# Kernel tuning notes

Measured on AMD Instinct MI355X. Metric: run time of the kernel, lower is better.

Reference implementation:

```python
import jax, jax.numpy as jnp
import numpy as np

N = 100000
E = 800000
F_IN = 256
HID = 64
H = 4
NEG_SLOPE = 0.2
BN_EPS = 1e-5


def setup_inputs() -> dict:
    key = jax.random.key(0)
    ks = jax.random.split(key, 20)
    s = 0.05
    return {
        "x": jax.random.normal(ks[0], (N, F_IN), jnp.float32),
        "edge_index": jax.random.randint(ks[1], (2, E), 0, N, jnp.int64),
        # GCNConv params
        "W_gcn": jax.random.normal(ks[2], (F_IN, HID), jnp.float32) * s,
        "b_gcn": jnp.zeros((HID,), jnp.float32),
        "g0": jnp.ones((HID,), jnp.float32),
        "beta0": jnp.zeros((HID,), jnp.float32),
        # GATConv 1 params
        "W1": jax.random.normal(ks[3], (HID, H * HID), jnp.float32) * s,
        "a_src1": jax.random.normal(ks[4], (H, HID), jnp.float32) * s,
        "a_dst1": jax.random.normal(ks[5], (H, HID), jnp.float32) * s,
        "b1": jnp.zeros((H * HID,), jnp.float32),
        "g1": jnp.ones((H * HID,), jnp.float32),
        "beta1": jnp.zeros((H * HID,), jnp.float32),
        # GATConv 2 params
        "W2": jax.random.normal(ks[6], (H * HID, H * HID), jnp.float32) * s,
        "a_src2": jax.random.normal(ks[7], (H, HID), jnp.float32) * s,
        "a_dst2": jax.random.normal(ks[8], (H, HID), jnp.float32) * s,
        "b2": jnp.zeros((H * HID,), jnp.float32),
        "g2": jnp.ones((H * HID,), jnp.float32),
        "beta2": jnp.zeros((H * HID,), jnp.float32),
    }


def _add_self_loops(edge_index, n):
    loop = jnp.arange(n, dtype=edge_index.dtype)
    src = jnp.concatenate([edge_index[0], loop])
    dst = jnp.concatenate([edge_index[1], loop])
    return src, dst


def _batch_norm(x, g, b):
    # BatchNorm1d, training-mode batch stats (biased variance), no dropout
    m = x.mean(0)
    v = x.var(0)
    return g * (x - m) * jax.lax.rsqrt(v + BN_EPS) + b


def _gcn_conv(x, src, dst, W, b, n):
    # symmetric normalization with self-loops already included in src/dst
    deg = jax.ops.segment_sum(jnp.ones_like(dst, jnp.float32), dst, n)
    dinv = jax.lax.rsqrt(jnp.maximum(deg, 1.0))
    norm = dinv[src] * dinv[dst]  # [E']
    h = x @ W  # [N, HID]
    out = jax.ops.segment_sum(h[src] * norm[:, None], dst, n)
    return out + b


def _gat_conv(x, src, dst, W, a_src, a_dst, b, n):
    h = (x @ W).reshape(n, H, HID)  # [N, H, C]
    alpha_s = jnp.einsum("nhc,hc->nh", h, a_src)  # [N, H]
    alpha_d = jnp.einsum("nhc,hc->nh", h, a_dst)
    e = alpha_s[src] + alpha_d[dst]  # [E', H]
    e = jnp.where(e > 0, e, NEG_SLOPE * e)  # LeakyReLU
    # softmax over incoming edges of each dst node, per head
    emax = jax.ops.segment_max(e, dst, n)
    w = jnp.exp(e - emax[dst])
    wsum = jax.ops.segment_sum(w, dst, n)
    att = w / wsum[dst]  # [E', H]
    out = jax.ops.segment_sum(att[:, :, None] * h[src], dst, n)  # [N, H, C]
    return out.reshape(n, H * HID) + b


def reference(x, edge_index, W_gcn, b_gcn, g0, beta0, W1, a_src1, a_dst1, b1,
              g1, beta1, W2, a_src2, a_dst2, b2, g2, beta2):
    n = x.shape[0]
    src, dst = _add_self_loops(edge_index, n)
    h = jax.nn.relu(_gcn_conv(x, src, dst, W_gcn, b_gcn, n))
    h = _batch_norm(h, g0, beta0)
    h = _gat_conv(h, src, dst, W1, a_src1, a_dst1, b1, n)
    h = jax.nn.elu(_batch_norm(h, g1, beta1))
    h = _gat_conv(h, src, dst, W2, a_src2, a_dst2, b2, n)
    h = jax.nn.elu(_batch_norm(h, g2, beta2))
    return h
```

## Files before the change

kernel.cpp:

```cpp
#include <hip/hip_runtime.h>
#include <hip/hip_bf16.h>
#include <math.h>

#define NN 100000
#define EE 800000
#define FIN 256
#define CH 64
#define C1 256
#define BN_EPS 1e-5f
#define NEG_SLOPE 0.2f

typedef __attribute__((ext_vector_type(8))) short short8;
typedef __attribute__((ext_vector_type(8))) unsigned short u16x8;
typedef __attribute__((ext_vector_type(4))) float f32x4;

__device__ __forceinline__ float bf2f(ushort u) {
    return __uint_as_float(((unsigned)u) << 16);
}
__device__ __forceinline__ ushort f2bf(float f) {
    unsigned u = __float_as_uint(f);
    return (ushort)((u + 0x7FFF + ((u >> 16) & 1)) >> 16);
}

__global__ void hist_kernel(const int* __restrict__ ei, int* __restrict__ deg) {
    int t = blockIdx.x * 256 + threadIdx.x;
    if (t < EE) atomicAdd(&deg[ei[EE + t]], 1);
}
__global__ void dinv_kernel(const int* __restrict__ deg, float* __restrict__ dinv) {
    int i = blockIdx.x * 256 + threadIdx.x;
    if (i < NN) dinv[i] = rsqrtf((float)(deg[i] + 1));
}
__global__ void scan_k1(const int* __restrict__ deg, int* __restrict__ row_start,
                        int* __restrict__ bsum) {
    __shared__ int sh[256];
    int t = threadIdx.x;
    int i = blockIdx.x * 256 + t;
    int v = (i < NN) ? (deg[i] + 1) : 0;
    sh[t] = v;
    __syncthreads();
    for (int off = 1; off < 256; off <<= 1) {
        int add = (t >= off) ? sh[t - off] : 0;
        __syncthreads();
        sh[t] += add;
        __syncthreads();
    }
    if (i < NN) row_start[i] = sh[t] - v;
    if (t == 255) bsum[blockIdx.x] = sh[255];
}
__global__ void scan_k2(int* __restrict__ bsum, int nb) {
    __shared__ int sh[512];
    int t = threadIdx.x;
    int v = (t < nb) ? bsum[t] : 0;
    sh[t] = v;
    __syncthreads();
    for (int off = 1; off < 512; off <<= 1) {
        int add = (t >= off) ? sh[t - off] : 0;
        __syncthreads();
        sh[t] += add;
        __syncthreads();
    }
    if (t < nb) bsum[t] = sh[t] - v;
}
__global__ void scan_k3(int* __restrict__ row_start, const int* __restrict__ bsum) {
    int i = blockIdx.x * 256 + threadIdx.x;
    if (i < NN) row_start[i] += bsum[i >> 8];
    if (i == NN) row_start[NN] = EE + NN;
}
__global__ void scatter_kernel(const int* __restrict__ ei, const int* __restrict__ row_start,
                               int* __restrict__ fill, int* __restrict__ sorted) {
    int t = blockIdx.x * 256 + threadIdx.x;
    if (t >= EE + NN) return;
    int s, d;
    if (t < EE) { s = ei[t]; d = ei[EE + t]; }
    else        { s = t - EE; d = s; }
    int pos = atomicAdd(&fill[d], 1);
    sorted[row_start[d] + pos] = s;
}

__global__ void transpose_w(const float* __restrict__ W, ushort* __restrict__ Bt, int M, int K) {
    int idx = blockIdx.x * 256 + threadIdx.x;
    if (idx < M * K) {
        int m = idx / K, n = idx % K;
        Bt[n * M + m] = f2bf(W[idx]);
    }
}

__global__ __launch_bounds__(256) void gemm_mfma(
        const void* __restrict__ Ap, const ushort* __restrict__ Bt,
        ushort* __restrict__ C, int M, int K, int a_fp32,
        const float* __restrict__ a_src, const float* __restrict__ a_dst,
        float* __restrict__ alpha_s, float* __restrict__ alpha_d) {
    __shared__ ushort As[64][40];
    __shared__ ushort Bs[64][40];
    int t = threadIdx.x;
    int w = t >> 6;
    int l = t & 63;
    int rowBase = blockIdx.y * 64;
    int colBase = blockIdx.x * 64;
    int srow = t >> 2;
    int sk = (t & 3) * 8;
    int m = l & 15, q = l >> 4;
    f32x4 acc[4] = {};
    for (int k0 = 0; k0 < M; k0 += 32) {
        int gr = rowBase + srow;
        if (a_fp32) {
            ushort4 u0 = {0, 0, 0, 0}, u1 = {0, 0, 0, 0};
            if (gr < NN) {
                const float* Af = (const float*)Ap;
                float4 f0 = *(const float4*)&Af[(long)gr * M + k0 + sk];
                float4 f1 = *(const float4*)&Af[(long)gr * M + k0 + sk + 4];
                u0.x = f2bf(f0.x); u0.y = f2bf(f0.y); u0.z = f2bf(f0.z); u0.w = f2bf(f0.w);
                u1.x = f2bf(f1.x); u1.y = f2bf(f1.y); u1.z = f2bf(f1.z); u1.w = f2bf(f1.w);
            }
            *(ushort4*)&As[srow][sk] = u0;
            *(ushort4*)&As[srow][sk + 4] = u1;
        } else {
            uint4 av = make_uint4(0u, 0u, 0u, 0u);
            if (gr < NN) av = *(const uint4*)&((const ushort*)Ap)[(long)gr * M + k0 + sk];
            *(uint4*)&As[srow][sk] = av;
        }
        uint4 bv = *(const uint4*)&Bt[(long)(colBase + srow) * M + k0 + sk];
        *(uint4*)&Bs[srow][sk] = bv;
        __syncthreads();
        short8 af = *(const short8*)&As[w * 16 + m][q * 8];
#pragma unroll
        for (int c = 0; c < 4; ++c) {
            short8 bf = *(const short8*)&Bs[c * 16 + m][q * 8];
            acc[c] = __builtin_amdgcn_mfma_f32_16x16x32_bf16(af, bf, acc[c], 0, 0, 0);
        }
        __syncthreads();
    }
    if (alpha_s) {
        int head = colBase >> 6;
        float ps[4] = {}, pd[4] = {};
#pragma unroll
        for (int c = 0; c < 4; ++c) {
            float av = a_src[colBase + c * 16 + m];
            float dv = a_dst[colBase + c * 16 + m];
#pragma unroll
            for (int r = 0; r < 4; ++r) {
                ps[r] += acc[c][r] * av;
                pd[r] += acc[c][r] * dv;
            }
        }
#pragma unroll
        for (int r = 0; r < 4; ++r) {
            ps[r] += __shfl_xor(ps[r], 1); pd[r] += __shfl_xor(pd[r], 1);
            ps[r] += __shfl_xor(ps[r], 2); pd[r] += __shfl_xor(pd[r], 2);
            ps[r] += __shfl_xor(ps[r], 4); pd[r] += __shfl_xor(pd[r], 4);
            ps[r] += __shfl_xor(ps[r], 8); pd[r] += __shfl_xor(pd[r], 8);
        }
        if (m == 0) {
#pragma unroll
            for (int r = 0; r < 4; ++r) {
                int row = rowBase + w * 16 + q * 4 + r;
                if (row < NN) {
                    alpha_s[row * 4 + head] = ps[r];
                    alpha_d[row * 4 + head] = pd[r];
                }
            }
        }
    }
#pragma unroll
    for (int c = 0; c < 4; ++c) {
#pragma unroll
        for (int r = 0; r < 4; ++r) {
            int orow = rowBase + w * 16 + q * 4 + r;
            if (orow < NN) C[(long)orow * K + colBase + c * 16 + m] = f2bf(acc[c][r]);
        }
    }
}

__global__ __launch_bounds__(256) void gcn_gather(
        const int* __restrict__ row_start, const int* __restrict__ sorted,
        const float* __restrict__ dinv, const ushort* __restrict__ h0,
        float* __restrict__ agg) {
    int node = blockIdx.x * 4 + (threadIdx.x >> 6);
    if (node >= NN) return;
    int l = threadIdx.x & 63;
    int slot = l >> 3;
    int li = l & 7;
    int c = li * 8;
    int b = row_start[node], e = row_start[node + 1];
    float a[8] = {};
    for (int i = b + slot; i < e; i += 8) {
        int s = sorted[i];
        float dv = dinv[s];
        u16x8 v = *(const u16x8*)&h0[(long)s * 64 + c];
#pragma unroll
        for (int j = 0; j < 8; ++j) a[j] += dv * bf2f((ushort)v[j]);
    }
#pragma unroll
    for (int j = 0; j < 8; ++j) {
        a[j] += __shfl_xor(a[j], 8);
        a[j] += __shfl_xor(a[j], 16);
        a[j] += __shfl_xor(a[j], 32);
    }
    if (slot == 0) {
        float dn = dinv[node];
        f32x4 o0, o1;
#pragma unroll
        for (int j = 0; j < 4; ++j) { o0[j] = a[j] * dn; o1[j] = a[4 + j] * dn; }
        *(f32x4*)&agg[(long)node * 64 + c] = o0;
        *(f32x4*)&agg[(long)node * 64 + c + 4] = o1;
    }
}

__global__ __launch_bounds__(256) void bn_stats64(
        const float* __restrict__ x, const float* __restrict__ bias,
        float* __restrict__ sums, float* __restrict__ sumsq) {
    __shared__ float red[4][16][8];
    int l = threadIdx.x & 63;
    int w = threadIdx.x >> 6;
    int wv = blockIdx.x * 4 + w;
    int nw = gridDim.x * 4;
    int sub = l >> 4;
    int c = (l & 15) * 4;
    f32x4 b4 = *(const f32x4*)&bias[c];
    float s0 = 0.f, s1 = 0.f, s2 = 0.f, s3 = 0.f;
    float q0 = 0.f, q1 = 0.f, q2 = 0.f, q3 = 0.f;
    for (int r = wv * 4 + sub; r < NN; r += nw * 4) {
        f32x4 v = *(const f32x4*)&x[(long)r * 64 + c];
        float v0 = fmaxf(v[0] + b4[0], 0.f);
        float v1 = fmaxf(v[1] + b4[1], 0.f);
        float v2 = fmaxf(v[2] + b4[2], 0.f);
        float v3 = fmaxf(v[3] + b4[3], 0.f);
        s0 += v0; s1 += v1; s2 += v2; s3 += v3;
        q0 += v0 * v0; q1 += v1 * v1; q2 += v2 * v2; q3 += v3 * v3;
    }
    s0 += __shfl_xor(s0, 16); s1 += __shfl_xor(s1, 16);
    s2 += __shfl_xor(s2, 16); s3 += __shfl_xor(s3, 16);
    q0 += __shfl_xor(q0, 16); q1 += __shfl_xor(q1, 16);
    q2 += __shfl_xor(q2, 16); q3 += __shfl_xor(q3, 16);
    s0 += __shfl_xor(s0, 32); s1 += __shfl_xor(s1, 32);
    s2 += __shfl_xor(s2, 32); s3 += __shfl_xor(s3, 32);
    q0 += __shfl_xor(q0, 32); q1 += __shfl_xor(q1, 32);
    q2 += __shfl_xor(q2, 32); q3 += __shfl_xor(q3, 32);
    if (sub == 0) {
        int li = l & 15;
        red[w][li][0] = s0; red[w][li][1] = s1; red[w][li][2] = s2; red[w][li][3] = s3;
        red[w][li][4] = q0; red[w][li][5] = q1; red[w][li][6] = q2; red[w][li][7] = q3;
    }
    __syncthreads();
    if (w == 0 && sub == 0) {
        int li = l & 15;
        atomicAdd(&sums[c + 0], red[0][li][0] + red[1][li][0] + red[2][li][0] + red[3][li][0]);
        atomicAdd(&sums[c + 1], red[0][li][1] + red[1][li][1] + red[2][li][1] + red[3][li][1]);
        atomicAdd(&sums[c + 2], red[0][li][2] + red[1][li][2] + red[2][li][2] + red[3][li][2]);
        atomicAdd(&sums[c + 3], red[0][li][3] + red[1][li][3] + red[2][li][3] + red[3][li][3]);
        atomicAdd(&sumsq[c + 0], red[0][li][4] + red[1][li][4] + red[2][li][4] + red[3][li][4]);
        atomicAdd(&sumsq[c + 1], red[0][li][5] + red[1][li][5] + red[2][li][5] + red[3][li][5]);
        atomicAdd(&sumsq[c + 2], red[0][li][6] + red[1][li][6] + red[2][li][6] + red[3][li][6]);
        atomicAdd(&sumsq[c + 3], red[0][li][7] + red[1][li][7] + red[2][li][7] + red[3][li][7]);
    }
}
__global__ __launch_bounds__(256) void bn_stats256(
        const ushort* __restrict__ x,
        float* __restrict__ sums, float* __restrict__ sumsq) {
    __shared__ float red[4][64][8];
    int l = threadIdx.x & 63;
    int w = threadIdx.x >> 6;
    int wv = blockIdx.x * 4 + w;
    int nw = gridDim.x * 4;
    int c = l * 4;
    float s0 = 0.f, s1 = 0.f, s2 = 0.f, s3 = 0.f;
    float q0 = 0.f, q1 = 0.f, q2 = 0.f, q3 = 0.f;
    for (int r = wv; r < NN; r += nw) {
        ushort4 v = *(const ushort4*)&x[(long)r * 256 + c];
        float v0 = bf2f(v.x), v1 = bf2f(v.y), v2 = bf2f(v.z), v3 = bf2f(v.w);
        s0 += v0; s1 += v1; s2 += v2; s3 += v3;
        q0 += v0 * v0; q1 += v1 * v1; q2 += v2 * v2; q3 += v3 * v3;
    }
    red[w][l][0] = s0; red[w][l][1] = s1; red[w][l][2] = s2; red[w][l][3] = s3;
    red[w][l][4] = q0; red[w][l][5] = q1; red[w][l][6] = q2; red[w][l][7] = q3;
    __syncthreads();
    if (w == 0) {
        atomicAdd(&sums[c + 0], red[0][l][0] + red[1][l][0] + red[2][l][0] + red[3][l][0]);
        atomicAdd(&sums[c + 1], red[0][l][1] + red[1][l][1] + red[2][l][1] + red[3][l][1]);
        atomicAdd(&sums[c + 2], red[0][l][2] + red[1][l][2] + red[2][l][2] + red[3][l][2]);
        atomicAdd(&sums[c + 3], red[0][l][3] + red[1][l][3] + red[2][l][3] + red[3][l][3]);
        atomicAdd(&sumsq[c + 0], red[0][l][4] + red[1][l][4] + red[2][l][4] + red[3][l][4]);
        atomicAdd(&sumsq[c + 1], red[0][l][5] + red[1][l][5] + red[2][l][5] + red[3][l][5]);
        atomicAdd(&sumsq[c + 2], red[0][l][6] + red[1][l][6] + red[2][l][6] + red[3][l][6]);
        atomicAdd(&sumsq[c + 3], red[0][l][7] + red[1][l][7] + red[2][l][7] + red[3][l][7]);
    }
}
__global__ void bn_finalize(const float* __restrict__ sums, const float* __restrict__ sumsq,
                            const float* __restrict__ g, const float* __restrict__ beta,
                            float* __restrict__ scale, float* __restrict__ shift, int C) {
    int c = threadIdx.x;
    if (c < C) {
        float mean = sums[c] / (float)NN;
        float var = sumsq[c] / (float)NN - mean * mean;
        float sc = g[c] * rsqrtf(var + BN_EPS);
        scale[c] = sc;
        shift[c] = beta[c] - mean * sc;
    }
}
__global__ __launch_bounds__(256) void bn_apply_gcn(
        const float* __restrict__ x, const float* __restrict__ bias,
        const float* __restrict__ scale, const float* __restrict__ shift,
        ushort* __restrict__ out) {
    int l = threadIdx.x & 63;
    int wv = blockIdx.x * 4 + (threadIdx.x >> 6);
    int nw = gridDim.x * 4;
    int c = (l & 15) * 4;
    int sub = l >> 4;
    f32x4 b4  = *(const f32x4*)&bias[c];
    f32x4 sc4 = *(const f32x4*)&scale[c];
    f32x4 sh4 = *(const f32x4*)&shift[c];
    for (int r = wv * 4 + sub; r < NN; r += nw * 4) {
        f32x4 v = *(const f32x4*)&x[(long)r * 64 + c];
        ushort4 o;
        o.x = f2bf(sc4[0] * fmaxf(v[0] + b4[0], 0.f) + sh4[0]);
        o.y = f2bf(sc4[1] * fmaxf(v[1] + b4[1], 0.f) + sh4[1]);
        o.z = f2bf(sc4[2] * fmaxf(v[2] + b4[2], 0.f) + sh4[2]);
        o.w = f2bf(sc4[3] * fmaxf(v[3] + b4[3], 0.f) + sh4[3]);
        *(ushort4*)&out[(long)r * 64 + c] = o;
    }
}
__global__ __launch_bounds__(256) void bn_apply_gat(
        const ushort* __restrict__ x,
        const float* __restrict__ scale, const float* __restrict__ shift,
        void* __restrict__ out, int out_bf16) {
    int l = threadIdx.x & 63;
    int wv = blockIdx.x * 4 + (threadIdx.x >> 6);
    int nw = gridDim.x * 4;
    int c = l * 4;
    f32x4 sc4 = *(const f32x4*)&scale[c];
    f32x4 sh4 = *(const f32x4*)&shift[c];
    if (out_bf16) {
        ushort* ob = (ushort*)out;
        for (int r = wv; r < NN; r += nw) {
            ushort4 v = *(const ushort4*)&x[(long)r * 256 + c];
            float t0 = sc4[0] * bf2f(v.x) + sh4[0];
            float t1 = sc4[1] * bf2f(v.y) + sh4[1];
            float t2 = sc4[2] * bf2f(v.z) + sh4[2];
            float t3 = sc4[3] * bf2f(v.w) + sh4[3];
            t0 = (t0 > 0.f) ? t0 : (__expf(t0) - 1.f);
            t1 = (t1 > 0.f) ? t1 : (__expf(t1) - 1.f);
            t2 = (t2 > 0.f) ? t2 : (__expf(t2) - 1.f);
            t3 = (t3 > 0.f) ? t3 : (__expf(t3) - 1.f);
            ushort4 o;
            o.x = f2bf(t0); o.y = f2bf(t1); o.z = f2bf(t2); o.w = f2bf(t3);
            *(ushort4*)&ob[(long)r * 256 + c] = o;
        }
    } else {
        float* of = (float*)out;
        for (int r = wv; r < NN; r += nw) {
            ushort4 v = *(const ushort4*)&x[(long)r * 256 + c];
            float t0 = sc4[0] * bf2f(v.x) + sh4[0];
            float t1 = sc4[1] * bf2f(v.y) + sh4[1];
            float t2 = sc4[2] * bf2f(v.z) + sh4[2];
            float t3 = sc4[3] * bf2f(v.w) + sh4[3];
            f32x4 o;
            o[0] = (t0 > 0.f) ? t0 : (__expf(t0) - 1.f);
            o[1] = (t1 > 0.f) ? t1 : (__expf(t1) - 1.f);
            o[2] = (t2 > 0.f) ? t2 : (__expf(t2) - 1.f);
            o[3] = (t3 > 0.f) ? t3 : (__expf(t3) - 1.f);
            *(f32x4*)&of[(long)r * 256 + c] = o;
        }
    }
}

__global__ __launch_bounds__(256) void gat_gather(
        const int* __restrict__ row_start, const int* __restrict__ sorted,
        const float* __restrict__ as, const float* __restrict__ ad,
        const ushort* __restrict__ h, ushort* __restrict__ out) {
    int node = blockIdx.x * 4 + (threadIdx.x >> 6);
    if (node >= NN) return;
    int l = threadIdx.x & 63;
    int head = l >> 4;
    int b = row_start[node], e = row_start[node + 1];
    float adn = ad[node * 4 + head];
    float a0 = 0.f, a1 = 0.f, a2 = 0.f, a3 = 0.f;
    float ls = 0.f;
    int i = b;
    for (; i + 3 < e; i += 4) {
        int s[4]; float ev[4]; ushort4 v[4];
#pragma unroll
        for (int j = 0; j < 4; ++j) s[j] = sorted[i + j];
#pragma unroll
        for (int j = 0; j < 4; ++j) ev[j] = as[s[j] * 4 + head];
#pragma unroll
        for (int j = 0; j < 4; ++j) v[j] = *(const ushort4*)&h[(long)s[j] * 256 + l * 4];
#pragma unroll
        for (int j = 0; j < 4; ++j) {
            float t = ev[j] + adn;
            t = (t > 0.f) ? t : NEG_SLOPE * t;
            float wt = __expf(t);
            ls += wt;
            a0 += wt * bf2f(v[j].x);
            a1 += wt * bf2f(v[j].y);
            a2 += wt * bf2f(v[j].z);
            a3 += wt * bf2f(v[j].w);
        }
    }
    for (; i < e; ++i) {
        int sv = sorted[i];
        float t = as[sv * 4 + head] + adn;
        t = (t > 0.f) ? t : NEG_SLOPE * t;
        float wt = __expf(t);
        ushort4 v0 = *(const ushort4*)&h[(long)sv * 256 + l * 4];
        ls += wt;
        a0 += wt * bf2f(v0.x);
        a1 += wt * bf2f(v0.y);
        a2 += wt * bf2f(v0.z);
        a3 += wt * bf2f(v0.w);
    }
    float inv = 1.0f / ls;
    ushort4 o;
    o.x = f2bf(a0 * inv);
    o.y = f2bf(a1 * inv);
    o.z = f2bf(a2 * inv);
    o.w = f2bf(a3 * inv);
    *(ushort4*)&out[(long)node * 256 + l * 4] = o;
}

extern "C" void kernel_launch(void* const* d_in, const int* in_sizes, int n_in,
                              void* d_out, int out_size, void* d_ws, size_t ws_size,
                              hipStream_t stream) {
    const float* x      = (const float*)d_in[0];
    const int*   ei     = (const int*)d_in[1];
    const float* W_gcn  = (const float*)d_in[2];
    const float* b_gcn  = (const float*)d_in[3];
    const float* g0     = (const float*)d_in[4];
    const float* beta0  = (const float*)d_in[5];
    const float* W1     = (const float*)d_in[6];
    const float* a_src1 = (const float*)d_in[7];
    const float* a_dst1 = (const float*)d_in[8];
    const float* b1     = (const float*)d_in[9];
    const float* g1     = (const float*)d_in[10];
    const float* beta1  = (const float*)d_in[11];
    const float* W2     = (const float*)d_in[12];
    const float* a_src2 = (const float*)d_in[13];
    const float* a_dst2 = (const float*)d_in[14];
    const float* b2     = (const float*)d_in[15];
    const float* g2     = (const float*)d_in[16];
    const float* beta2  = (const float*)d_in[17];

    const long N = NN;
    float* ws = (float*)d_ws;

    float* dinv    = ws;
    float* alpha_s = ws + N;
    float* alpha_d = ws + 5 * N;
    float* sums    = ws + 9 * N;
    float* sumsq   = sums + 256;
    float* scale   = sumsq + 256;
    float* shift   = scale + 256;
    int*   row_start = (int*)(shift + 256);
    int*   fill      = row_start + NN + 1;
    int*   deg_i     = fill + NN;
    int*   sorted    = deg_i + NN;
    int*   bsum      = sorted + EE + NN;
    ushort* Wgt  = (ushort*)(ws + 23 * N);
    ushort* W1t  = Wgt + 16384;
    ushort* W2t  = W1t + 16384;
    ushort* h0b  = (ushort*)(ws + 24 * N);
    ushort* x1b  = h0b;
    float*  agg0 = ws + 56 * N;
    ushort* h1b  = (ushort*)(ws + 120 * N);
    ushort* x2b  = (ushort*)(ws + 248 * N);
    ushort* yb   = (ushort*)(ws + 376 * N);
    float*  outp = (float*)d_out;

    const int BLK = 256;
    dim3 blk(BLK);
    const int NBLK_N = (NN + 255) / 256;

    hipMemsetAsync(fill, 0, 2L * NN * sizeof(int), stream);
    hist_kernel<<<(EE + 255) / 256, blk, 0, stream>>>(ei, deg_i);
    dinv_kernel<<<NBLK_N, blk, 0, stream>>>(deg_i, dinv);
    scan_k1<<<NBLK_N, blk, 0, stream>>>(deg_i, row_start, bsum);
    scan_k2<<<1, 512, 0, stream>>>(bsum, NBLK_N);
    scan_k3<<<(NN + 1 + 255) / 256, blk, 0, stream>>>(row_start, bsum);
    scatter_kernel<<<(EE + NN + 255) / 256, blk, 0, stream>>>(ei, row_start, fill, sorted);

    transpose_w<<<(FIN * CH + 255) / 256, blk, 0, stream>>>(W_gcn, Wgt, FIN, CH);
    transpose_w<<<(CH * C1 + 255) / 256, blk, 0, stream>>>(W1, W1t, CH, C1);
    transpose_w<<<(C1 * C1 + 255) / 256, blk, 0, stream>>>(W2, W2t, C1, C1);

    gemm_mfma<<<dim3(CH / 64, (NN + 63) / 64), blk, 0, stream>>>(
        x, Wgt, h0b, FIN, CH, 1, nullptr, nullptr, nullptr, nullptr);
    gcn_gather<<<(NN + 3) / 4, blk, 0, stream>>>(row_start, sorted, dinv, h0b, agg0);
    hipMemsetAsync(sums, 0, 512 * sizeof(float), stream);
    bn_stats64<<<512, blk, 0, stream>>>(agg0, b_gcn, sums, sumsq);
    bn_finalize<<<1, CH, 0, stream>>>(sums, sumsq, g0, beta0, scale, shift, CH);
    bn_apply_gcn<<<1024, blk, 0, stream>>>(agg0, b_gcn, scale, shift, x1b);

    gemm_mfma<<<dim3(C1 / 64, (NN + 63) / 64), blk, 0, stream>>>(
        x1b, W1t, h1b, CH, C1, 0, a_src1, a_dst1, alpha_s, alpha_d);
    gat_gather<<<(NN + 3) / 4, blk, 0, stream>>>(row_start, sorted, alpha_s, alpha_d, h1b, yb);
    hipMemsetAsync(sums, 0, 512 * sizeof(float), stream);
    bn_stats256<<<512, blk, 0, stream>>>(yb, sums, sumsq);
    bn_finalize<<<1, C1, 0, stream>>>(sums, sumsq, g1, beta1, scale, shift, C1);
    bn_apply_gat<<<2048, blk, 0, stream>>>(yb, scale, shift, x2b, 1);

    gemm_mfma<<<dim3(C1 / 64, (NN + 63) / 64), blk, 0, stream>>>(
        x2b, W2t, h1b, C1, C1, 0, a_src2, a_dst2, alpha_s, alpha_d);
    gat_gather<<<(NN + 3) / 4, blk, 0, stream>>>(row_start, sorted, alpha_s, alpha_d, h1b, yb);
    hipMemsetAsync(sums, 0, 512 * sizeof(float), stream);
    bn_stats256<<<512, blk, 0, stream>>>(yb, sums, sumsq);
    bn_finalize<<<1, C1, 0, stream>>>(sums, sumsq, g2, beta2, scale, shift, C1);
    bn_apply_gat<<<2048, blk, 0, stream>>>(yb, scale, shift, outp, 0);
}
```

Baseline: 786.3 us.

## Fuse BN-apply activations into GEMM A-loads and merge small setup kernels

The GCN bias+ReLU+BN and the GAT1 BN+ELU are now applied while the next GEMM loads its A tile, so the two standalone bn_apply passes and their bf16 intermediate buffers go away. The dinv computation moves into the first scan kernel, the three weight transposes merge into one launch, and the three BN stat buffers are zeroed with one memset. This removes several kernel launches and a full read/write of 100k×64 and 100k×256 activations. In exchange, each GEMM A element is transformed once per column block: four times for the 256-wide outputs, including extra expf work in the layer-3 GEMM.

```diff
diff --git a/kernel.cpp b/kernel.cpp
--- a/kernel.cpp
+++ b/kernel.cpp
@@ -26,16 +26,13 @@
     int t = blockIdx.x * 256 + threadIdx.x;
     if (t < EE) atomicAdd(&deg[ei[EE + t]], 1);
 }
-__global__ void dinv_kernel(const int* __restrict__ deg, float* __restrict__ dinv) {
-    int i = blockIdx.x * 256 + threadIdx.x;
-    if (i < NN) dinv[i] = rsqrtf((float)(deg[i] + 1));
-}
 __global__ void scan_k1(const int* __restrict__ deg, int* __restrict__ row_start,
-                        int* __restrict__ bsum) {
+                        int* __restrict__ bsum, float* __restrict__ dinv) {
     __shared__ int sh[256];
     int t = threadIdx.x;
     int i = blockIdx.x * 256 + t;
     int v = (i < NN) ? (deg[i] + 1) : 0;
+    if (i < NN) dinv[i] = rsqrtf((float)v);
     sh[t] = v;
     __syncthreads();
     for (int off = 1; off < 256; off <<= 1) {
@@ -77,17 +74,30 @@
     sorted[row_start[d] + pos] = s;
 }
 
-__global__ void transpose_w(const float* __restrict__ W, ushort* __restrict__ Bt, int M, int K) {
+__global__ void transpose_all(const float* __restrict__ Wg, const float* __restrict__ W1,
+                              const float* __restrict__ W2, ushort* __restrict__ Wgt,
+                              ushort* __restrict__ W1t, ushort* __restrict__ W2t) {
     int idx = blockIdx.x * 256 + threadIdx.x;
-    if (idx < M * K) {
-        int m = idx / K, n = idx % K;
-        Bt[n * M + m] = f2bf(W[idx]);
-    }
-}
-
+    if (idx < FIN * CH) {
+        int m = idx / CH, n = idx % CH;
+        Wgt[n * FIN + m] = f2bf(Wg[idx]);
+    } else if (idx < FIN * CH + CH * C1) {
+        int i = idx - FIN * CH;
+        int m = i / C1, n = i % C1;
+        W1t[n * CH + m] = f2bf(W1[i]);
+    } else if (idx < FIN * CH + CH * C1 + C1 * C1) {
+        int i = idx - FIN * CH - CH * C1;
+        int m = i / C1, n = i % C1;
+        W2t[n * C1 + m] = f2bf(W2[i]);
+    }
+}
+
+template<int AMODE>
 __global__ __launch_bounds__(256) void gemm_mfma(
         const void* __restrict__ Ap, const ushort* __restrict__ Bt,
-        ushort* __restrict__ C, int M, int K, int a_fp32,
+        ushort* __restrict__ C, int M, int K,
+        const float* __restrict__ t_bias, const float* __restrict__ t_scale,
+        const float* __restrict__ t_shift,
         const float* __restrict__ a_src, const float* __restrict__ a_dst,
         float* __restrict__ alpha_s, float* __restrict__ alpha_d) {
     __shared__ ushort As[64][40];
@@ -103,22 +113,53 @@
     f32x4 acc[4] = {};
     for (int k0 = 0; k0 < M; k0 += 32) {
         int gr = rowBase + srow;
-        if (a_fp32) {
-            ushort4 u0 = {0, 0, 0, 0}, u1 = {0, 0, 0, 0};
+        int ch = k0 + sk;
+        ushort4 u0 = {0, 0, 0, 0}, u1 = {0, 0, 0, 0};
+        if (AMODE == 1) {
             if (gr < NN) {
                 const float* Af = (const float*)Ap;
-                float4 f0 = *(const float4*)&Af[(long)gr * M + k0 + sk];
-                float4 f1 = *(const float4*)&Af[(long)gr * M + k0 + sk + 4];
+                float4 f0 = *(const float4*)&Af[(long)gr * M + ch];
+                float4 f1 = *(const float4*)&Af[(long)gr * M + ch + 4];
                 u0.x = f2bf(f0.x); u0.y = f2bf(f0.y); u0.z = f2bf(f0.z); u0.w = f2bf(f0.w);
                 u1.x = f2bf(f1.x); u1.y = f2bf(f1.y); u1.z = f2bf(f1.z); u1.w = f2bf(f1.w);
             }
-            *(ushort4*)&As[srow][sk] = u0;
-            *(ushort4*)&As[srow][sk + 4] = u1;
+        } else if (AMODE == 2) {
+            if (gr < NN) {
+                const float* Af = (const float*)Ap;
+                float4 f0 = *(const float4*)&Af[(long)gr * M + ch];
+                float4 f1 = *(const float4*)&Af[(long)gr * M + ch + 4];
+                f32x4 b0 = *(const f32x4*)&t_bias[ch],  b1 = *(const f32x4*)&t_bias[ch + 4];
+                f32x4 s0 = *(const f32x4*)&t_scale[ch], s1 = *(const f32x4*)&t_scale[ch + 4];
+                f32x4 h0 = *(const f32x4*)&t_shift[ch], h1 = *(const f32x4*)&t_shift[ch + 4];
+                u0.x = f2bf(s0[0] * fmaxf(f0.x + b0[0], 0.f) + h0[0]);
+                u0.y = f2bf(s0[1] * fmaxf(f0.y + b0[1], 0.f) + h0[1]);
+                u0.z = f2bf(s0[2] * fmaxf(f0.z + b0[2], 0.f) + h0[2]);
+                u0.w = f2bf(s0[3] * fmaxf(f0.w + b0[3], 0.f) + h0[3]);
+                u1.x = f2bf(s1[0] * fmaxf(f1.x + b1[0], 0.f) + h1[0]);
+                u1.y = f2bf(s1[1] * fmaxf(f1.y + b1[1], 0.f) + h1[1]);
+                u1.z = f2bf(s1[2] * fmaxf(f1.z + b1[2], 0.f) + h1[2]);
+                u1.w = f2bf(s1[3] * fmaxf(f1.w + b1[3], 0.f) + h1[3]);
+            }
         } else {
-            uint4 av = make_uint4(0u, 0u, 0u, 0u);
-            if (gr < NN) av = *(const uint4*)&((const ushort*)Ap)[(long)gr * M + k0 + sk];
-            *(uint4*)&As[srow][sk] = av;
-        }
+            if (gr < NN) {
+                const ushort* Ab = (const ushort*)Ap;
+                u16x8 y = *(const u16x8*)&Ab[(long)gr * M + ch];
+                f32x4 s0 = *(const f32x4*)&t_scale[ch], s1 = *(const f32x4*)&t_scale[ch + 4];
+                f32x4 h0 = *(const f32x4*)&t_shift[ch], h1 = *(const f32x4*)&t_shift[ch + 4];
+                float r[8];
+#pragma unroll
+                for (int j = 0; j < 8; ++j) {
+                    float sc = (j < 4) ? s0[j] : s1[j - 4];
+                    float sh = (j < 4) ? h0[j] : h1[j - 4];
+                    float v = sc * bf2f((ushort)y[j]) + sh;
+                    r[j] = (v > 0.f) ? v : (__expf(v) - 1.f);
+                }
+                u0.x = f2bf(r[0]); u0.y = f2bf(r[1]); u0.z = f2bf(r[2]); u0.w = f2bf(r[3]);
+                u1.x = f2bf(r[4]); u1.y = f2bf(r[5]); u1.z = f2bf(r[6]); u1.w = f2bf(r[7]);
+            }
+        }
+        *(ushort4*)&As[srow][sk] = u0;
+        *(ushort4*)&As[srow][sk + 4] = u1;
         uint4 bv = *(const uint4*)&Bt[(long)(colBase + srow) * M + k0 + sk];
         *(uint4*)&Bs[srow][sk] = bv;
         __syncthreads();
@@ -297,69 +338,28 @@
         shift[c] = beta[c] - mean * sc;
     }
 }
-__global__ __launch_bounds__(256) void bn_apply_gcn(
-        const float* __restrict__ x, const float* __restrict__ bias,
-        const float* __restrict__ scale, const float* __restrict__ shift,
-        ushort* __restrict__ out) {
-    int l = threadIdx.x & 63;
-    int wv = blockIdx.x * 4 + (threadIdx.x >> 6);
-    int nw = gridDim.x * 4;
-    int c = (l & 15) * 4;
-    int sub = l >> 4;
-    f32x4 b4  = *(const f32x4*)&bias[c];
-    f32x4 sc4 = *(const f32x4*)&scale[c];
-    f32x4 sh4 = *(const f32x4*)&shift[c];
-    for (int r = wv * 4 + sub; r < NN; r += nw * 4) {
-        f32x4 v = *(const f32x4*)&x[(long)r * 64 + c];
-        ushort4 o;
-        o.x = f2bf(sc4[0] * fmaxf(v[0] + b4[0], 0.f) + sh4[0]);
-        o.y = f2bf(sc4[1] * fmaxf(v[1] + b4[1], 0.f) + sh4[1]);
-        o.z = f2bf(sc4[2] * fmaxf(v[2] + b4[2], 0.f) + sh4[2]);
-        o.w = f2bf(sc4[3] * fmaxf(v[3] + b4[3], 0.f) + sh4[3]);
-        *(ushort4*)&out[(long)r * 64 + c] = o;
-    }
-}
 __global__ __launch_bounds__(256) void bn_apply_gat(
         const ushort* __restrict__ x,
         const float* __restrict__ scale, const float* __restrict__ shift,
-        void* __restrict__ out, int out_bf16) {
+        float* __restrict__ out) {
     int l = threadIdx.x & 63;
     int wv = blockIdx.x * 4 + (threadIdx.x >> 6);
     int nw = gridDim.x * 4;
     int c = l * 4;
     f32x4 sc4 = *(const f32x4*)&scale[c];
     f32x4 sh4 = *(const f32x4*)&shift[c];
-    if (out_bf16) {
-        ushort* ob = (ushort*)out;
-        for (int r = wv; r < NN; r += nw) {
-            ushort4 v = *(const ushort4*)&x[(long)r * 256 + c];
-            float t0 = sc4[0] * bf2f(v.x) + sh4[0];
-            float t1 = sc4[1] * bf2f(v.y) + sh4[1];
-            float t2 = sc4[2] * bf2f(v.z) + sh4[2];
-            float t3 = sc4[3] * bf2f(v.w) + sh4[3];
-            t0 = (t0 > 0.f) ? t0 : (__expf(t0) - 1.f);
-            t1 = (t1 > 0.f) ? t1 : (__expf(t1) - 1.f);
-            t2 = (t2 > 0.f) ? t2 : (__expf(t2) - 1.f);
-            t3 = (t3 > 0.f) ? t3 : (__expf(t3) - 1.f);
-            ushort4 o;
-            o.x = f2bf(t0); o.y = f2bf(t1); o.z = f2bf(t2); o.w = f2bf(t3);
-            *(ushort4*)&ob[(long)r * 256 + c] = o;
-        }
-    } else {
-        float* of = (float*)out;
-        for (int r = wv; r < NN; r += nw) {
-            ushort4 v = *(const ushort4*)&x[(long)r * 256 + c];
-            float t0 = sc4[0] * bf2f(v.x) + sh4[0];
-            float t1 = sc4[1] * bf2f(v.y) + sh4[1];
-            float t2 = sc4[2] * bf2f(v.z) + sh4[2];
-            float t3 = sc4[3] * bf2f(v.w) + sh4[3];
-            f32x4 o;
-            o[0] = (t0 > 0.f) ? t0 : (__expf(t0) - 1.f);
-            o[1] = (t1 > 0.f) ? t1 : (__expf(t1) - 1.f);
-            o[2] = (t2 > 0.f) ? t2 : (__expf(t2) - 1.f);
-            o[3] = (t3 > 0.f) ? t3 : (__expf(t3) - 1.f);
-            *(f32x4*)&of[(long)r * 256 + c] = o;
-        }
+    for (int r = wv; r < NN; r += nw) {
+        ushort4 v = *(const ushort4*)&x[(long)r * 256 + c];
+        float t0 = sc4[0] * bf2f(v.x) + sh4[0];
+        float t1 = sc4[1] * bf2f(v.y) + sh4[1];
+        float t2 = sc4[2] * bf2f(v.z) + sh4[2];
+        float t3 = sc4[3] * bf2f(v.w) + sh4[3];
+        f32x4 o;
+        o[0] = (t0 > 0.f) ? t0 : (__expf(t0) - 1.f);
+        o[1] = (t1 > 0.f) ? t1 : (__expf(t1) - 1.f);
+        o[2] = (t2 > 0.f) ? t2 : (__expf(t2) - 1.f);
+        o[3] = (t3 > 0.f) ? t3 : (__expf(t3) - 1.f);
+        *(f32x4*)&out[(long)r * 256 + c] = o;
     }
 }
 
@@ -445,9 +445,13 @@
     float* dinv    = ws;
     float* alpha_s = ws + N;
     float* alpha_d = ws + 5 * N;
-    float* sums    = ws + 9 * N;
-    float* sumsq   = sums + 256;
-    float* scale   = sumsq + 256;
+    float* sums0   = ws + 9 * N;
+    float* sumsq0  = sums0 + 64;
+    float* sums1   = sumsq0 + 64;
+    float* sumsq1  = sums1 + 256;
+    float* sums2   = sumsq1 + 256;
+    float* sumsq2  = sums2 + 256;
+    float* scale   = sumsq2 + 256;
     float* shift   = scale + 256;
     int*   row_start = (int*)(shift + 256);
     int*   fill      = row_start + NN + 1;
@@ -458,10 +462,8 @@
     ushort* W1t  = Wgt + 16384;
     ushort* W2t  = W1t + 16384;
     ushort* h0b  = (ushort*)(ws + 24 * N);
-    ushort* x1b  = h0b;
     float*  agg0 = ws + 56 * N;
     ushort* h1b  = (ushort*)(ws + 120 * N);
-    ushort* x2b  = (ushort*)(ws + 248 * N);
     ushort* yb   = (ushort*)(ws + 376 * N);
     float*  outp = (float*)d_out;
 
@@ -470,38 +472,35 @@
     const int NBLK_N = (NN + 255) / 256;
 
     hipMemsetAsync(fill, 0, 2L * NN * sizeof(int), stream);
+    hipMemsetAsync(sums0, 0, 1152 * sizeof(float), stream);
     hist_kernel<<<(EE + 255) / 256, blk, 0, stream>>>(ei, deg_i);
-    dinv_kernel<<<NBLK_N, blk, 0, stream>>>(deg_i, dinv);
-    scan_k1<<<NBLK_N, blk, 0, stream>>>(deg_i, row_start, bsum);
+    scan_k1<<<NBLK_N, blk, 0, stream>>>(deg_i, row_start, bsum, dinv);
     scan_k2<<<1, 512, 0, stream>>>(bsum, NBLK_N);
     scan_k3<<<(NN + 1 + 255) / 256, blk, 0, stream>>>(row_start, bsum);
     scatter_kernel<<<(EE + NN + 255) / 256, blk, 0, stream>>>(ei, row_start, fill, sorted);
 
-    transpose_w<<<(FIN * CH + 255) / 256, blk, 0, stream>>>(W_gcn, Wgt, FIN, CH);
-    transpose_w<<<(CH * C1 + 255) / 256, blk, 0, stream>>>(W1, W1t, CH, C1);
-    transpose_w<<<(C1 * C1 + 255) / 256, blk, 0, stream>>>(W2, W2t, C1, C1);
-
-    gemm_mfma<<<dim3(CH / 64, (NN + 63) / 64), blk, 0, stream>>>(
-        x, Wgt, h0b, FIN, CH, 1, nullptr, nullptr, nullptr, nullptr);
+    transpose_all<<<(FIN * CH + CH * C1 + C1 * C1 + 255) / 256, blk, 0, stream>>>(
+        W_gcn, W1, W2, Wgt, W1t, W2t);
+
+    gemm_mfma<1><<<dim3(CH / 64, (NN + 63) / 64), blk, 0, stream>>>(
+        x, Wgt, h0b, FIN, CH, nullptr, nullptr, nullptr,
+        nullptr, nullptr, nullptr, nullptr);
     gcn_gather<<<(NN + 3) / 4, blk, 0, stream>>>(row_start, sorted, dinv, h0b, agg0);
-    hipMemsetAsync(sums, 0, 512 * sizeof(float), stream);
-    bn_stats64<<<512, blk, 0, stream>>>(agg0, b_gcn, sums, sumsq);
-    bn_finalize<<<1, CH, 0, stream>>>(sums, sumsq, g0, beta0, scale, shift, CH);
-    bn_apply_gcn<<<1024, blk, 0, stream>>>(agg0, b_gcn, scale, shift, x1b);
-
-    gemm_mfma<<<dim3(C1 / 64, (NN + 63) / 64), blk, 0, stream>>>(
-        x1b, W1t, h1b, CH, C1, 0, a_src1, a_dst1, alpha_s, alpha_d);
+    bn_stats64<<<512, blk, 0, stream>>>(agg0, b_gcn, sums0, sumsq0);
+    bn_finalize<<<1, CH, 0, stream>>>(sums0, sumsq0, g0, beta0, scale, shift, CH);
+
+    gemm_mfma<2><<<dim3(C1 / 64, (NN + 63) / 64), blk, 0, stream>>>(
+        agg0, W1t, h1b, CH, C1, b_gcn, scale, shift,
+        a_src1, a_dst1, alpha_s, alpha_d);
     gat_gather<<<(NN + 3) / 4, blk, 0, stream>>>(row_start, sorted, alpha_s, alpha_d, h1b, yb);
-    hipMemsetAsync(sums, 0, 512 * sizeof(float), stream);
-    bn_stats256<<<512, blk, 0, stream>>>(yb, sums, sumsq);
-    bn_finalize<<<1, C1, 0, stream>>>(sums, sumsq, g1, beta1, scale, shift, C1);
-    bn_apply_gat<<<2048, blk, 0, stream>>>(yb, scale, shift, x2b, 1);
-
-    gemm_mfma<<<dim3(C1 / 64, (NN + 63) / 64), blk, 0, stream>>>(
-        x2b, W2t, h1b, C1, C1, 0, a_src2, a_dst2, alpha_s, alpha_d);
+    bn_stats256<<<512, blk, 0, stream>>>(yb, sums1, sumsq1);
+    bn_finalize<<<1, C1, 0, stream>>>(sums1, sumsq1, g1, beta1, scale, shift, C1);
+
+    gemm_mfma<3><<<dim3(C1 / 64, (NN + 63) / 64), blk, 0, stream>>>(
+        yb, W2t, h1b, C1, C1, nullptr, scale, shift,
+        a_src2, a_dst2, alpha_s, alpha_d);
     gat_gather<<<(NN + 3) / 4, blk, 0, stream>>>(row_start, sorted, alpha_s, alpha_d, h1b, yb);
-    hipMemsetAsync(sums, 0, 512 * sizeof(float), stream);
-    bn_stats256<<<512, blk, 0, stream>>>(yb, sums, sumsq);
-    bn_finalize<<<1, C1, 0, stream>>>(sums, sumsq, g2, beta2, scale, shift, C1);
-    bn_apply_gat<<<2048, blk, 0, stream>>>(yb, scale, shift, outp, 0);
-}
+    bn_stats256<<<512, blk, 0, stream>>>(yb, sums2, sumsq2);
+    bn_finalize<<<1, C1, 0, stream>>>(sums2, sumsq2, g2, beta2, scale, shift, C1);
+    bn_apply_gat<<<2048, blk, 0, stream>>>(yb, scale, shift, outp);
+}
```

Result: no change. 792.1 us (+0.7%).
